# Kernel tuning notes

Measured on AMD Instinct MI355X. Metric: run time of the kernel, lower is better.

## Reference

```python
import jax, jax.numpy as jnp
import numpy as np

H = 8      # num_attention_heads
DH = 96    # attention_head_size
LN_EPS = 1e-5


def setup_inputs() -> dict:
    key = jax.random.key(0)
    ks = jax.random.split(key, 12)
    B, S, D = 2, 768, 768
    sc = 0.02
    return {
        "hidden_states": jax.random.normal(ks[0], (B, S, D), jnp.float32),
        "distance_matrix": jax.random.uniform(ks[1], (B, S, S), jnp.float32) * 20.0,
        "angle_matrix": jax.random.uniform(ks[2], (B, S, S), jnp.float32) * np.pi,
        "attention_mask": jnp.ones((B, S), jnp.float32),
        "Wq": jax.random.normal(ks[3], (D, D), jnp.float32) * sc,
        "bq": jnp.zeros((D,), jnp.float32),
        "Wk": jax.random.normal(ks[4], (D, D), jnp.float32) * sc,
        "bk": jnp.zeros((D,), jnp.float32),
        "Wv": jax.random.normal(ks[5], (D, D), jnp.float32) * sc,
        "bv": jnp.zeros((D,), jnp.float32),
        "Wd": jax.random.normal(ks[6], (DH,), jnp.float32) * sc,
        "bd": jnp.zeros((DH,), jnp.float32),
        "Wa": jax.random.normal(ks[7], (DH,), jnp.float32) * sc,
        "ba": jnp.zeros((DH,), jnp.float32),
        "Wo": jax.random.normal(ks[8], (D, D), jnp.float32) * sc,
        "bo": jnp.zeros((D,), jnp.float32),
        "ln_g": jnp.ones((D,), jnp.float32),
        "ln_b": jnp.zeros((D,), jnp.float32),
    }


def _heads(x, B, S):
    # [B,S,D] -> [B,H,S,DH]
    return x.reshape(B, S, H, DH).transpose(0, 2, 1, 3)


def reference(hidden_states, distance_matrix, angle_matrix, attention_mask,
              Wq, bq, Wk, bk, Wv, bv, Wd, bd, Wa, ba, Wo, bo, ln_g, ln_b):
    B, S, D = hidden_states.shape
    q = _heads(hidden_states @ Wq.T + bq, B, S)   # [B,H,S,DH]
    k = _heads(hidden_states @ Wk.T + bk, B, S)
    v = _heads(hidden_states @ Wv.T + bv, B, S)

    scores = jnp.einsum('bhid,bhjd->bhij', q, k) / jnp.sqrt(jnp.float32(DH))

    # distance / angle relative-position biases: emb[b,i,j,:] = dist[b,i,j]*Wd + bd
    dist_emb = distance_matrix[..., None] * Wd + bd   # [B,S,S,DH]
    scores = scores + jnp.einsum('bhid,bijd->bhij', q, dist_emb)
    ang_emb = angle_matrix[..., None] * Wa + ba       # [B,S,S,DH]
    scores = scores + jnp.einsum('bhid,bijd->bhij', q, ang_emb)

    # key mask, broadcast over heads and query positions
    scores = scores + (1.0 - attention_mask)[:, None, None, :] * -10000.0

    probs = jax.nn.softmax(scores, axis=-1)           # [B,H,S,S]
    ctx = jnp.einsum('bhij,bhjd->bhid', probs, v)
    ctx = ctx.transpose(0, 2, 1, 3).reshape(B, S, D)  # [B,S,D]

    out = ctx @ Wo.T + bo
    x = out + hidden_states
    mu = jnp.mean(x, axis=-1, keepdims=True)
    var = jnp.var(x, axis=-1, keepdims=True)
    out = (x - mu) * jax.lax.rsqrt(var + LN_EPS) * ln_g + ln_b
    return out, probs
```

## Files before the change

### kernel.cpp

```cpp
#include <hip/hip_runtime.h>
#include <stdint.h>

#define B_  2
#define S_  768
#define D_  768
#define H_  8
#define DH_ 96

typedef unsigned short ushort_t;
typedef __bf16 bf16x8 __attribute__((ext_vector_type(8)));
typedef float  f32x4  __attribute__((ext_vector_type(4)));
typedef _Float16 f16x4 __attribute__((ext_vector_type(4)));

__device__ inline ushort_t f2bf(float f) {
    union { float f; unsigned int u; } v; v.f = f;
    unsigned int u = v.u;
    unsigned int r = u + 0x7fffu + ((u >> 16) & 1u);
    return (ushort_t)(r >> 16);
}
__device__ inline float bf2f(ushort_t u) {
    union { unsigned int i; float f; } c; c.i = ((unsigned int)u) << 16;
    return c.f;
}
__device__ inline ushort_t f2h(float f) {
    union { _Float16 h; ushort_t u; } c; c.h = (_Float16)f; return c.u;
}

__device__ inline void glds16(const void* gp, void* lp) {
    auto g = reinterpret_cast<const __attribute__((address_space(1))) uint32_t*>(
        reinterpret_cast<uintptr_t>(gp));
    auto l = reinterpret_cast<__attribute__((address_space(3))) uint32_t*>(
        reinterpret_cast<uintptr_t>(lp));
    __builtin_amdgcn_global_load_lds(g, l, 16, 0, 0);
}

#define SBAR()  { __builtin_amdgcn_sched_barrier(0); __builtin_amdgcn_s_barrier(); \
                  __builtin_amdgcn_sched_barrier(0); }
#define WAIT_VM(N) { asm volatile("s_waitcnt vmcnt(" #N ")" ::: "memory"); \
                     __builtin_amdgcn_sched_barrier(0); }
#define WAIT_LGKM0() { asm volatile("s_waitcnt lgkmcnt(0)" ::: "memory"); \
                       __builtin_amdgcn_sched_barrier(0); }

__global__ __launch_bounds__(256) void k_convert(
        const float* __restrict__ X, const float* __restrict__ Wq,
        const float* __restrict__ Wk, const float* __restrict__ Wv,
        const float* __restrict__ Wo, const float* __restrict__ distm,
        const float* __restrict__ angm,
        ushort_t* __restrict__ Xb, ushort_t* __restrict__ Wb,
        ushort_t* __restrict__ Dh, ushort_t* __restrict__ Ah) {
    __shared__ float tlds[64][65];
    const int NX4 = (B_ * S_ * D_) / 4;
    const int NW4 = (D_ * D_) / 4;
    const int bid = blockIdx.x, tid = threadIdx.x;
    if (bid < 3456) {
        int i = bid * 256 + tid;
        float4 v;
        ushort_t* dst;
        if (i < NX4) {
            v = ((const float4*)X)[i];
            dst = Xb + i * 4;
        } else {
            int wi = i - NX4;
            int sel = wi / NW4;
            int off = wi - sel * NW4;
            const float* src = (sel == 0) ? Wq : (sel == 1) ? Wk : (sel == 2) ? Wv : Wo;
            v = ((const float4*)src)[off];
            dst = Wb + wi * 4;
        }
        ushort4 o;
        o.x = f2bf(v.x); o.y = f2bf(v.y); o.z = f2bf(v.z); o.w = f2bf(v.w);
        *(ushort4*)dst = o;
        return;
    }
    int tidx = bid - 3456;
    int mat = tidx / 288, t2 = tidx - mat * 288;
    int b = t2 / 144, t3 = t2 - b * 144;
    int rt = t3 / 12, ct = t3 - rt * 12;
    const float* src = (mat ? angm : distm) + ((size_t)(b * S_ + rt * 64)) * S_ + ct * 64;
    ushort_t* dstm = mat ? Ah : Dh;
    {
        int tr = tid >> 4, tc4 = tid & 15;
        #pragma unroll
        for (int k = 0; k < 4; ++k) {
            int row = tr + k * 16;
            float4 v4 = *(const float4*)(src + (size_t)row * S_ + tc4 * 4);
            tlds[row][tc4 * 4 + 0] = v4.x;
            tlds[row][tc4 * 4 + 1] = v4.y;
            tlds[row][tc4 * 4 + 2] = v4.z;
            tlds[row][tc4 * 4 + 3] = v4.w;
        }
    }
    __syncthreads();
    {
        int row = tid & 63, s4b = tid >> 6;
        #pragma unroll
        for (int k = 0; k < 4; ++k) {
            int s4l = s4b * 4 + k;
            ushort4 o4;
            o4.x = f2h(tlds[row][s4l * 4 + 0]);
            o4.y = f2h(tlds[row][s4l * 4 + 1]);
            o4.z = f2h(tlds[row][s4l * 4 + 2]);
            o4.w = f2h(tlds[row][s4l * 4 + 3]);
            *(ushort4*)&dstm[(((size_t)b * 192 + ct * 16 + s4l) * 768 + rt * 64 + row) * 4] = o4;
        }
    }
}

__device__ inline void gemm64_dbuf(
        const ushort_t* __restrict__ A, int lda,
        const ushort_t* __restrict__ Bt, int ldb,
        int K, int m0, int n0,
        ushort_t* As, ushort_t* Bs, f32x4 acc[2][2]) {
    const int tid  = threadIdx.x;
    const int lane = tid & 63, wave = tid >> 6;
    const int wm = (wave >> 1) * 32, wn = (wave & 1) * 32;
    const int fr = lane & 15, fk = (lane >> 4) * 8;
    const ushort_t* Ap = A  + (size_t)(m0 + wave * 16 + (lane >> 2)) * lda + (lane & 3) * 8;
    const ushort_t* Bp = Bt + (size_t)(n0 + wave * 16 + (lane >> 2)) * ldb + (lane & 3) * 8;
    glds16(Ap, As + wave * 512);
    glds16(Bp, Bs + wave * 512);
    for (int kt = 0; kt < K; kt += 32) {
        const int cur = (kt >> 5) & 1;
        if (kt + 32 < K) {
            glds16(Ap + kt + 32, As + (cur ^ 1) * 2048 + wave * 512);
            glds16(Bp + kt + 32, Bs + (cur ^ 1) * 2048 + wave * 512);
            WAIT_VM(2)
        } else {
            WAIT_VM(0)
        }
        SBAR()
        const ushort_t* Ab = As + cur * 2048;
        const ushort_t* Bb = Bs + cur * 2048;
        bf16x8 a0 = *(const bf16x8*)&Ab[(wm      + fr) * 32 + fk];
        bf16x8 a1 = *(const bf16x8*)&Ab[(wm + 16 + fr) * 32 + fk];
        bf16x8 b0 = *(const bf16x8*)&Bb[(wn      + fr) * 32 + fk];
        bf16x8 b1 = *(const bf16x8*)&Bb[(wn + 16 + fr) * 32 + fk];
        acc[0][0] = __builtin_amdgcn_mfma_f32_16x16x32_bf16(a0, b0, acc[0][0], 0, 0, 0);
        acc[0][1] = __builtin_amdgcn_mfma_f32_16x16x32_bf16(a0, b1, acc[0][1], 0, 0, 0);
        acc[1][0] = __builtin_amdgcn_mfma_f32_16x16x32_bf16(a1, b0, acc[1][0], 0, 0, 0);
        acc[1][1] = __builtin_amdgcn_mfma_f32_16x16x32_bf16(a1, b1, acc[1][1], 0, 0, 0);
        WAIT_LGKM0()
        SBAR()
    }
}

__global__ __launch_bounds__(256) void k_qkv(
        const ushort_t* __restrict__ Xb, const ushort_t* __restrict__ Wb,
        const float* __restrict__ bq, const float* __restrict__ bk,
        const float* __restrict__ bv,
        ushort_t* __restrict__ Qb, ushort_t* __restrict__ Kb,
        ushort_t* __restrict__ Vtb) {
    __shared__ __align__(16) ushort_t As[2 * 64 * 32];
    __shared__ __align__(16) ushort_t Bs[2 * 64 * 32];
    f32x4 acc[2][2];
    #pragma unroll
    for (int i = 0; i < 2; i++)
        #pragma unroll
        for (int j = 0; j < 2; j++) acc[i][j] = (f32x4){0.f, 0.f, 0.f, 0.f};
    const int m0 = blockIdx.y * 64, n0 = blockIdx.x * 64;
    gemm64_dbuf(Xb, D_, Wb, D_, D_, m0, n0, As, Bs, acc);
    const int lane = threadIdx.x & 63, wave = threadIdx.x >> 6;
    const int wm = (wave >> 1) * 32, wn = (wave & 1) * 32;
    #pragma unroll
    for (int ni = 0; ni < 2; ni++) {
        int gcol = n0 + wn + ni * 16 + (lane & 15);
        int gsel = gcol / D_, d768 = gcol - gsel * D_;
        int h = d768 / DH_, d = d768 - h * DH_;
        float bias = (gsel == 0 ? bq : (gsel == 1 ? bk : bv))[d768];
        #pragma unroll
        for (int mi = 0; mi < 2; mi++) {
            int grow0 = m0 + wm + mi * 16 + (lane >> 4) * 4;
            int b = grow0 / S_, s0 = grow0 - b * S_;
            int bh = b * H_ + h;
            if (gsel == 2) {
                ushort4 o4;
                o4.x = f2bf(acc[mi][ni][0] + bias);
                o4.y = f2bf(acc[mi][ni][1] + bias);
                o4.z = f2bf(acc[mi][ni][2] + bias);
                o4.w = f2bf(acc[mi][ni][3] + bias);
                int p = s0 >> 7, wv = (s0 >> 4) & 3, gq = (s0 >> 2) & 3;
                int e0 = (s0 >> 6) & 1;
                size_t off = ((size_t)bh * 73728) + p * 12288 + wv * 3072
                           + (d >> 4) * 512 + (gq * 16 + (d & 15)) * 8 + e0 * 4;
                *(ushort4*)&Vtb[off] = o4;
            } else if (gsel == 1) {
                #pragma unroll
                for (int r = 0; r < 4; r++)
                    Kb[(((size_t)bh * 12 + (d >> 3)) * S_ + s0 + r) * 8 + (d & 7)] =
                        f2bf(acc[mi][ni][r] + bias);
            } else {
                #pragma unroll
                for (int r = 0; r < 4; r++)
                    Qb[((size_t)bh * S_ + s0 + r) * DH_ + d] = f2bf(acc[mi][ni][r] + bias);
            }
        }
    }
}

__global__ __launch_bounds__(256, 3) void k_flash(
        const ushort_t* __restrict__ Qb, const ushort_t* __restrict__ Kb,
        const ushort_t* __restrict__ Vtb,
        const float* __restrict__ Wd, const float* __restrict__ bd,
        const float* __restrict__ Wa, const float* __restrict__ ba,
        const ushort_t* __restrict__ Dh, const ushort_t* __restrict__ Ah,
        const float* __restrict__ mask,
        float* __restrict__ probs, ushort_t* __restrict__ Ctxb) {
    __shared__ float mstat[64];
    __shared__ float lstat[64];
    __shared__ float ctxred[1600];
    const int idx = blockIdx.x;
    const int bh = idx & 15, t = idx >> 4;
    const int b = bh >> 3, h = bh & 7;
    const int r0 = t * 16;
    const int tid = threadIdx.x, lane = tid & 63, w = tid >> 6;
    const int frn = lane & 15, g = lane >> 4;
    const ushort_t* Qbh = Qb + (size_t)bh * S_ * DH_;
    const ushort_t* Kbh = Kb + (size_t)bh * 12 * S_ * 8;

    #pragma unroll
    for (int i = 0; i < 7; ++i) {
        int z = tid + i * 256;
        if (z < 1600) ctxred[z] = 0.f;
    }

    bf16x8 aq0, aq1, aq2;
    {
        const ushort_t* qp = Qbh + (size_t)(r0 + frn) * DH_ + g * 8;
        aq0 = *(const bf16x8*)qp;
        aq1 = *(const bf16x8*)(qp + 32);
        aq2 = *(const bf16x8*)(qp + 64);
    }
    float qc0 = 0.f, qc1 = 0.f, qc2 = 0.f;
    #pragma unroll
    for (int f = 0; f < 3; ++f) {
        bf16x8 aq = (f == 0) ? aq0 : (f == 1) ? aq1 : aq2;
        #pragma unroll
        for (int e = 0; e < 8; ++e) {
            int d = f * 32 + g * 8 + e;
            float qv = (float)aq[e];
            qc0 += qv * Wd[d];
            qc1 += qv * Wa[d];
            qc2 += qv * (bd[d] + ba[d]);
        }
    }
    qc0 += __shfl_xor(qc0, 16); qc0 += __shfl_xor(qc0, 32);
    qc1 += __shfl_xor(qc1, 16); qc1 += __shfl_xor(qc1, 32);
    qc2 += __shfl_xor(qc2, 16); qc2 += __shfl_xor(qc2, 32);

    const float isq = 0.10206207261596577f;

    f32x4 acc[12];
    const ushort_t* kbase = Kbh + ((size_t)g * S_ + 16 * w + frn) * 8;
    const ushort_t* dbase = Dh + ((size_t)(b * 192 + w * 4 + g) * 768 + r0 + frn) * 4;
    const ushort_t* abase = Ah + ((size_t)(b * 192 + w * 4 + g) * 768 + r0 + frn) * 4;
    const float*    mbase = mask + b * S_ + w * 16 + g * 4;
    #pragma unroll
    for (int c = 0; c < 12; ++c) {
        const ushort_t* kp = kbase + (size_t)c * 64 * 8;
        bf16x8 k0 = *(const bf16x8*)kp;
        bf16x8 k1 = *(const bf16x8*)(kp + (size_t)4 * S_ * 8);
        bf16x8 k2 = *(const bf16x8*)(kp + (size_t)8 * S_ * 8);
        union { uint2 u; f16x4 hh; } dd, aa;
        dd.u = *(const uint2*)(dbase + (size_t)c * 16 * 768 * 4);
        aa.u = *(const uint2*)(abase + (size_t)c * 16 * 768 * 4);
        float4 m4 = *(const float4*)(mbase + c * 64);
        f32x4 ca = (f32x4){0.f, 0.f, 0.f, 0.f};
        ca = __builtin_amdgcn_mfma_f32_16x16x32_bf16(k0, aq0, ca, 0, 0, 0);
        ca = __builtin_amdgcn_mfma_f32_16x16x32_bf16(k1, aq1, ca, 0, 0, 0);
        ca = __builtin_amdgcn_mfma_f32_16x16x32_bf16(k2, aq2, ca, 0, 0, 0);
        f32x4 o;
        o[0] = ca[0] * isq + (float)dd.hh[0] * qc0 + (float)aa.hh[0] * qc1 + qc2 + (1.f - m4.x) * -10000.f;
        o[1] = ca[1] * isq + (float)dd.hh[1] * qc0 + (float)aa.hh[1] * qc1 + qc2 + (1.f - m4.y) * -10000.f;
        o[2] = ca[2] * isq + (float)dd.hh[2] * qc0 + (float)aa.hh[2] * qc1 + qc2 + (1.f - m4.z) * -10000.f;
        o[3] = ca[3] * isq + (float)dd.hh[3] * qc0 + (float)aa.hh[3] * qc1 + qc2 + (1.f - m4.w) * -10000.f;
        acc[c] = o;
    }

    float mx = -1e30f;
    #pragma unroll
    for (int c = 0; c < 12; ++c)
        #pragma unroll
        for (int r = 0; r < 4; ++r) mx = fmaxf(mx, acc[c][r]);
    mx = fmaxf(mx, __shfl_xor(mx, 16));
    mx = fmaxf(mx, __shfl_xor(mx, 32));
    if (g == 0) mstat[w * 16 + frn] = mx;
    __syncthreads();
    float mf = fmaxf(fmaxf(mstat[frn], mstat[16 + frn]),
                     fmaxf(mstat[32 + frn], mstat[48 + frn]));
    float sum = 0.f;
    #pragma unroll
    for (int c = 0; c < 12; ++c)
        #pragma unroll
        for (int r = 0; r < 4; ++r) {
            float e = __expf(acc[c][r] - mf);
            acc[c][r] = e;
            sum += e;
        }
    sum += __shfl_xor(sum, 16);
    sum += __shfl_xor(sum, 32);
    if (g == 0) lstat[w * 16 + frn] = sum;
    __syncthreads();
    float inv = 1.f / (lstat[frn] + lstat[16 + frn] + lstat[32 + frn] + lstat[48 + frn]);

    f32x4 accO[6];
    #pragma unroll
    for (int i = 0; i < 6; ++i) accO[i] = (f32x4){0.f, 0.f, 0.f, 0.f};
    float* prow = probs + ((size_t)bh * S_ + r0 + frn) * S_ + w * 16 + g * 4;
    const ushort_t* vfb = Vtb + (size_t)bh * 73728 + w * 3072 + lane * 8;
    #pragma unroll
    for (int p = 0; p < 6; ++p) {
        const int c = 2 * p;
        bf16x8 vfrag[6];
        #pragma unroll
        for (int nt = 0; nt < 6; ++nt)
            vfrag[nt] = *(const bf16x8*)(vfb + p * 12288 + nt * 512);
        float4 pw;
        pw.x = acc[c][0] * inv; pw.y = acc[c][1] * inv;
        pw.z = acc[c][2] * inv; pw.w = acc[c][3] * inv;
        *(float4*)(prow + c * 64) = pw;
        pw.x = acc[c + 1][0] * inv; pw.y = acc[c + 1][1] * inv;
        pw.z = acc[c + 1][2] * inv; pw.w = acc[c + 1][3] * inv;
        *(float4*)(prow + (c + 1) * 64) = pw;
        union { bf16x8 v; ushort_t u[8]; } pa;
        #pragma unroll
        for (int r = 0; r < 4; ++r) {
            pa.u[r]     = f2bf(acc[c][r]);
            pa.u[r + 4] = f2bf(acc[c + 1][r]);
        }
        #pragma unroll
        for (int nt = 0; nt < 6; ++nt)
            accO[nt] = __builtin_amdgcn_mfma_f32_16x16x32_bf16(pa.v, vfrag[nt], accO[nt], 0, 0, 0);
    }

    #pragma unroll
    for (int nt = 0; nt < 6; ++nt)
        #pragma unroll
        for (int r = 0; r < 4; ++r)
            atomicAdd(&ctxred[(4 * g + r) * 100 + nt * 16 + frn], accO[nt][r]);
    __syncthreads();
    {
        int zr = tid >> 4, zc = tid & 15;
        float ivr = 1.f / (lstat[zr] + lstat[16 + zr] + lstat[32 + zr] + lstat[48 + zr]);
        ushort_t* crow = Ctxb + ((size_t)b * S_ + r0 + zr) * D_ + h * DH_;
        #pragma unroll
        for (int i = 0; i < 6; ++i)
            crow[i * 16 + zc] = f2bf(ctxred[zr * 100 + i * 16 + zc] * ivr);
    }
}

__global__ __launch_bounds__(256) void k_out(
        const ushort_t* __restrict__ Ctxb, const ushort_t* __restrict__ Wob,
        const float* __restrict__ bo, const float* __restrict__ hidden,
        float* __restrict__ xbuf) {
    __shared__ __align__(16) ushort_t As[2 * 64 * 32];
    __shared__ __align__(16) ushort_t Bs[2 * 64 * 32];
    f32x4 acc[2][2];
    #pragma unroll
    for (int i = 0; i < 2; i++)
        #pragma unroll
        for (int j = 0; j < 2; j++) acc[i][j] = (f32x4){0.f, 0.f, 0.f, 0.f};
    const int m0 = blockIdx.y * 64, n0 = blockIdx.x * 64;
    gemm64_dbuf(Ctxb, D_, Wob, D_, D_, m0, n0, As, Bs, acc);
    const int lane = threadIdx.x & 63, wave = threadIdx.x >> 6;
    const int wm = (wave >> 1) * 32, wn = (wave & 1) * 32;
    #pragma unroll
    for (int ni = 0; ni < 2; ni++) {
        int gcol = n0 + wn + ni * 16 + (lane & 15);
        float bias = bo[gcol];
        #pragma unroll
        for (int mi = 0; mi < 2; mi++) {
            #pragma unroll
            for (int r = 0; r < 4; r++) {
                int grow = m0 + wm + mi * 16 + (lane >> 4) * 4 + r;
                xbuf[(size_t)grow * D_ + gcol] =
                    acc[mi][ni][r] + bias + hidden[(size_t)grow * D_ + gcol];
            }
        }
    }
}

__global__ __launch_bounds__(256) void k_ln(
        const float* __restrict__ xbuf, const float* __restrict__ g,
        const float* __restrict__ bb, float* __restrict__ out) {
    const float* x = xbuf + (size_t)blockIdx.x * D_;
    const int t = threadIdx.x;
    float a0 = x[t], a1 = x[t + 256], a2 = x[t + 512];
    float s = a0 + a1 + a2;
    float ss = a0 * a0 + a1 * a1 + a2 * a2;
    __shared__ float r1[4], r2[4];
    #pragma unroll
    for (int o = 32; o > 0; o >>= 1) { s += __shfl_down(s, o); ss += __shfl_down(ss, o); }
    if ((t & 63) == 0) { r1[t >> 6] = s; r2[t >> 6] = ss; }
    __syncthreads();
    float ts = r1[0] + r1[1] + r1[2] + r1[3];
    float tss = r2[0] + r2[1] + r2[2] + r2[3];
    float mu = ts * (1.0f / D_);
    float var = tss * (1.0f / D_) - mu * mu;
    float rstd = rsqrtf(var + 1e-5f);
    float* o = out + (size_t)blockIdx.x * D_;
    o[t]       = (a0 - mu) * rstd * g[t]       + bb[t];
    o[t + 256] = (a1 - mu) * rstd * g[t + 256] + bb[t + 256];
    o[t + 512] = (a2 - mu) * rstd * g[t + 512] + bb[t + 512];
}

extern "C" void kernel_launch(void* const* d_in, const int* in_sizes, int n_in,
                              void* d_out, int out_size, void* d_ws, size_t ws_size,
                              hipStream_t stream) {
    const float* X     = (const float*)d_in[0];
    const float* distm = (const float*)d_in[1];
    const float* angm  = (const float*)d_in[2];
    const float* mask  = (const float*)d_in[3];
    const float* Wq    = (const float*)d_in[4];
    const float* bq    = (const float*)d_in[5];
    const float* Wk    = (const float*)d_in[6];
    const float* bk    = (const float*)d_in[7];
    const float* Wv    = (const float*)d_in[8];
    const float* bv    = (const float*)d_in[9];
    const float* Wd    = (const float*)d_in[10];
    const float* bd    = (const float*)d_in[11];
    const float* Wa    = (const float*)d_in[12];
    const float* ba    = (const float*)d_in[13];
    const float* Wo    = (const float*)d_in[14];
    const float* bo    = (const float*)d_in[15];
    const float* ln_g  = (const float*)d_in[16];
    const float* ln_b  = (const float*)d_in[17];

    float* outp  = (float*)d_out;
    float* probs = (float*)d_out + (size_t)B_ * S_ * D_;

    char* ws = (char*)d_ws;
    ushort_t* Xb    = (ushort_t*)(ws + 0);
    ushort_t* Wb    = (ushort_t*)(ws + 2359296);
    ushort_t* Qb    = (ushort_t*)(ws + 7077888);
    ushort_t* Kb    = (ushort_t*)(ws + 9437184);
    ushort_t* Vtb   = (ushort_t*)(ws + 11796480);
    ushort_t* Ctxb  = (ushort_t*)(ws + 14155776);
    float*    xbuf  = (float*)   (ws + 16662528);
    ushort_t* Dh    = (ushort_t*)(ws + 16662528);
    ushort_t* Ah    = (ushort_t*)(ws + 16662528 + 2359296);

    k_convert<<<4032, 256, 0, stream>>>(X, Wq, Wk, Wv, Wo, distm, angm, Xb, Wb, Dh, Ah);
    k_qkv<<<dim3(36, 24), 256, 0, stream>>>(Xb, Wb, bq, bk, bv, Qb, Kb, Vtb);
    k_flash<<<768, 256, 0, stream>>>(Qb, Kb, Vtb, Wd, bd, Wa, ba, Dh, Ah, mask, probs, Ctxb);
    k_out<<<dim3(12, 24), 256, 0, stream>>>(Ctxb, Wb + (size_t)2304 * 768, bo, X, xbuf);
    k_ln<<<1536, 256, 0, stream>>>(xbuf, ln_g, ln_b, outp);
}
```

Before: 182.5 us.

## Triple-buffer GEMM LDS staging and software-prefetch K/V fragments in attention

The shared GEMM helper moves from double to triple buffering in LDS. The next-next tile is issued after a single barrier, which removes the second per-iteration barrier and the lgkmcnt wait. The attention kernel now prefetches the K, distance, angle and mask fragments two chunks ahead and V fragments one chunk ahead in registers, and writes the probs output with nontemporal stores. The intent is to hide global-memory latency and reduce sync overhead, at the cost of more LDS and registers, which may lower occupancy.

```diff
diff --git a/kernel.cpp b/kernel.cpp
--- a/kernel.cpp
+++ b/kernel.cpp
@@ -38,8 +38,6 @@
                   __builtin_amdgcn_sched_barrier(0); }
 #define WAIT_VM(N) { asm volatile("s_waitcnt vmcnt(" #N ")" ::: "memory"); \
                      __builtin_amdgcn_sched_barrier(0); }
-#define WAIT_LGKM0() { asm volatile("s_waitcnt lgkmcnt(0)" ::: "memory"); \
-                       __builtin_amdgcn_sched_barrier(0); }
 
 __global__ __launch_bounds__(256) void k_convert(
         const float* __restrict__ X, const float* __restrict__ Wq,
@@ -106,7 +104,7 @@
     }
 }
 
-__device__ inline void gemm64_dbuf(
+__device__ inline void gemm64_tbuf(
         const ushort_t* __restrict__ A, int lda,
         const ushort_t* __restrict__ Bt, int ldb,
         int K, int m0, int n0,
@@ -117,18 +115,19 @@
     const int fr = lane & 15, fk = (lane >> 4) * 8;
     const ushort_t* Ap = A  + (size_t)(m0 + wave * 16 + (lane >> 2)) * lda + (lane & 3) * 8;
     const ushort_t* Bp = Bt + (size_t)(n0 + wave * 16 + (lane >> 2)) * ldb + (lane & 3) * 8;
-    glds16(Ap, As + wave * 512);
-    glds16(Bp, Bs + wave * 512);
+    glds16(Ap,      As + wave * 512);
+    glds16(Bp,      Bs + wave * 512);
+    glds16(Ap + 32, As + 2048 + wave * 512);
+    glds16(Bp + 32, Bs + 2048 + wave * 512);
     for (int kt = 0; kt < K; kt += 32) {
-        const int cur = (kt >> 5) & 1;
-        if (kt + 32 < K) {
-            glds16(Ap + kt + 32, As + (cur ^ 1) * 2048 + wave * 512);
-            glds16(Bp + kt + 32, Bs + (cur ^ 1) * 2048 + wave * 512);
-            WAIT_VM(2)
-        } else {
-            WAIT_VM(0)
-        }
+        const int cur = (kt >> 5) % 3;
+        if (kt + 32 < K) { WAIT_VM(2) } else { WAIT_VM(0) }
         SBAR()
+        if (kt + 64 < K) {
+            const int nb = ((kt >> 5) + 2) % 3;
+            glds16(Ap + kt + 64, As + nb * 2048 + wave * 512);
+            glds16(Bp + kt + 64, Bs + nb * 2048 + wave * 512);
+        }
         const ushort_t* Ab = As + cur * 2048;
         const ushort_t* Bb = Bs + cur * 2048;
         bf16x8 a0 = *(const bf16x8*)&Ab[(wm      + fr) * 32 + fk];
@@ -139,8 +138,6 @@
         acc[0][1] = __builtin_amdgcn_mfma_f32_16x16x32_bf16(a0, b1, acc[0][1], 0, 0, 0);
         acc[1][0] = __builtin_amdgcn_mfma_f32_16x16x32_bf16(a1, b0, acc[1][0], 0, 0, 0);
         acc[1][1] = __builtin_amdgcn_mfma_f32_16x16x32_bf16(a1, b1, acc[1][1], 0, 0, 0);
-        WAIT_LGKM0()
-        SBAR()
     }
 }
 
@@ -150,15 +147,15 @@
         const float* __restrict__ bv,
         ushort_t* __restrict__ Qb, ushort_t* __restrict__ Kb,
         ushort_t* __restrict__ Vtb) {
-    __shared__ __align__(16) ushort_t As[2 * 64 * 32];
-    __shared__ __align__(16) ushort_t Bs[2 * 64 * 32];
+    __shared__ __align__(16) ushort_t As[3 * 64 * 32];
+    __shared__ __align__(16) ushort_t Bs[3 * 64 * 32];
     f32x4 acc[2][2];
     #pragma unroll
     for (int i = 0; i < 2; i++)
         #pragma unroll
         for (int j = 0; j < 2; j++) acc[i][j] = (f32x4){0.f, 0.f, 0.f, 0.f};
     const int m0 = blockIdx.y * 64, n0 = blockIdx.x * 64;
-    gemm64_dbuf(Xb, D_, Wb, D_, D_, m0, n0, As, Bs, acc);
+    gemm64_tbuf(Xb, D_, Wb, D_, D_, m0, n0, As, Bs, acc);
     const int lane = threadIdx.x & 63, wave = threadIdx.x >> 6;
     const int wm = (wave >> 1) * 32, wn = (wave & 1) * 32;
     #pragma unroll
@@ -254,26 +251,36 @@
     const ushort_t* dbase = Dh + ((size_t)(b * 192 + w * 4 + g) * 768 + r0 + frn) * 4;
     const ushort_t* abase = Ah + ((size_t)(b * 192 + w * 4 + g) * 768 + r0 + frn) * 4;
     const float*    mbase = mask + b * S_ + w * 16 + g * 4;
+    struct Ch { bf16x8 k0, k1, k2; uint2 dd, aa; float4 m4; };
+    auto LDC = [&](int c) {
+        Ch r;
+        const ushort_t* kp = kbase + (size_t)c * 64 * 8;
+        r.k0 = *(const bf16x8*)kp;
+        r.k1 = *(const bf16x8*)(kp + (size_t)4 * S_ * 8);
+        r.k2 = *(const bf16x8*)(kp + (size_t)8 * S_ * 8);
+        r.dd = *(const uint2*)(dbase + (size_t)c * 16 * 768 * 4);
+        r.aa = *(const uint2*)(abase + (size_t)c * 16 * 768 * 4);
+        r.m4 = *(const float4*)(mbase + c * 64);
+        return r;
+    };
+    Ch p0 = LDC(0), p1 = LDC(1);
     #pragma unroll
     for (int c = 0; c < 12; ++c) {
-        const ushort_t* kp = kbase + (size_t)c * 64 * 8;
-        bf16x8 k0 = *(const bf16x8*)kp;
-        bf16x8 k1 = *(const bf16x8*)(kp + (size_t)4 * S_ * 8);
-        bf16x8 k2 = *(const bf16x8*)(kp + (size_t)8 * S_ * 8);
+        Ch nx;
+        if (c < 10) nx = LDC(c + 2); else nx = p1;
+        f32x4 ca = (f32x4){0.f, 0.f, 0.f, 0.f};
+        ca = __builtin_amdgcn_mfma_f32_16x16x32_bf16(p0.k0, aq0, ca, 0, 0, 0);
+        ca = __builtin_amdgcn_mfma_f32_16x16x32_bf16(p0.k1, aq1, ca, 0, 0, 0);
+        ca = __builtin_amdgcn_mfma_f32_16x16x32_bf16(p0.k2, aq2, ca, 0, 0, 0);
         union { uint2 u; f16x4 hh; } dd, aa;
-        dd.u = *(const uint2*)(dbase + (size_t)c * 16 * 768 * 4);
-        aa.u = *(const uint2*)(abase + (size_t)c * 16 * 768 * 4);
-        float4 m4 = *(const float4*)(mbase + c * 64);
-        f32x4 ca = (f32x4){0.f, 0.f, 0.f, 0.f};
-        ca = __builtin_amdgcn_mfma_f32_16x16x32_bf16(k0, aq0, ca, 0, 0, 0);
-        ca = __builtin_amdgcn_mfma_f32_16x16x32_bf16(k1, aq1, ca, 0, 0, 0);
-        ca = __builtin_amdgcn_mfma_f32_16x16x32_bf16(k2, aq2, ca, 0, 0, 0);
+        dd.u = p0.dd; aa.u = p0.aa;
         f32x4 o;
-        o[0] = ca[0] * isq + (float)dd.hh[0] * qc0 + (float)aa.hh[0] * qc1 + qc2 + (1.f - m4.x) * -10000.f;
-        o[1] = ca[1] * isq + (float)dd.hh[1] * qc0 + (float)aa.hh[1] * qc1 + qc2 + (1.f - m4.y) * -10000.f;
-        o[2] = ca[2] * isq + (float)dd.hh[2] * qc0 + (float)aa.hh[2] * qc1 + qc2 + (1.f - m4.z) * -10000.f;
-        o[3] = ca[3] * isq + (float)dd.hh[3] * qc0 + (float)aa.hh[3] * qc1 + qc2 + (1.f - m4.w) * -10000.f;
+        o[0] = ca[0] * isq + (float)dd.hh[0] * qc0 + (float)aa.hh[0] * qc1 + qc2 + (1.f - p0.m4.x) * -10000.f;
+        o[1] = ca[1] * isq + (float)dd.hh[1] * qc0 + (float)aa.hh[1] * qc1 + qc2 + (1.f - p0.m4.y) * -10000.f;
+        o[2] = ca[2] * isq + (float)dd.hh[2] * qc0 + (float)aa.hh[2] * qc1 + qc2 + (1.f - p0.m4.z) * -10000.f;
+        o[3] = ca[3] * isq + (float)dd.hh[3] * qc0 + (float)aa.hh[3] * qc1 + qc2 + (1.f - p0.m4.w) * -10000.f;
         acc[c] = o;
+        p0 = p1; p1 = nx;
     }
 
     float mx = -1e30f;
@@ -307,20 +314,25 @@
     for (int i = 0; i < 6; ++i) accO[i] = (f32x4){0.f, 0.f, 0.f, 0.f};
     float* prow = probs + ((size_t)bh * S_ + r0 + frn) * S_ + w * 16 + g * 4;
     const ushort_t* vfb = Vtb + (size_t)bh * 73728 + w * 3072 + lane * 8;
+    bf16x8 vcur[6];
+    #pragma unroll
+    for (int nt = 0; nt < 6; ++nt)
+        vcur[nt] = *(const bf16x8*)(vfb + nt * 512);
     #pragma unroll
     for (int p = 0; p < 6; ++p) {
         const int c = 2 * p;
-        bf16x8 vfrag[6];
+        bf16x8 vnx[6];
         #pragma unroll
         for (int nt = 0; nt < 6; ++nt)
-            vfrag[nt] = *(const bf16x8*)(vfb + p * 12288 + nt * 512);
-        float4 pw;
-        pw.x = acc[c][0] * inv; pw.y = acc[c][1] * inv;
-        pw.z = acc[c][2] * inv; pw.w = acc[c][3] * inv;
-        *(float4*)(prow + c * 64) = pw;
-        pw.x = acc[c + 1][0] * inv; pw.y = acc[c + 1][1] * inv;
-        pw.z = acc[c + 1][2] * inv; pw.w = acc[c + 1][3] * inv;
-        *(float4*)(prow + (c + 1) * 64) = pw;
+            vnx[nt] = (p < 5) ? *(const bf16x8*)(vfb + (p + 1) * 12288 + nt * 512)
+                              : vcur[nt];
+        f32x4 pw;
+        pw[0] = acc[c][0] * inv; pw[1] = acc[c][1] * inv;
+        pw[2] = acc[c][2] * inv; pw[3] = acc[c][3] * inv;
+        __builtin_nontemporal_store(pw, (f32x4*)(prow + c * 64));
+        pw[0] = acc[c + 1][0] * inv; pw[1] = acc[c + 1][1] * inv;
+        pw[2] = acc[c + 1][2] * inv; pw[3] = acc[c + 1][3] * inv;
+        __builtin_nontemporal_store(pw, (f32x4*)(prow + (c + 1) * 64));
         union { bf16x8 v; ushort_t u[8]; } pa;
         #pragma unroll
         for (int r = 0; r < 4; ++r) {
@@ -329,7 +341,9 @@
         }
         #pragma unroll
         for (int nt = 0; nt < 6; ++nt)
-            accO[nt] = __builtin_amdgcn_mfma_f32_16x16x32_bf16(pa.v, vfrag[nt], accO[nt], 0, 0, 0);
+            accO[nt] = __builtin_amdgcn_mfma_f32_16x16x32_bf16(pa.v, vcur[nt], accO[nt], 0, 0, 0);
+        #pragma unroll
+        for (int nt = 0; nt < 6; ++nt) vcur[nt] = vnx[nt];
     }
 
     #pragma unroll
@@ -352,15 +366,15 @@
         const ushort_t* __restrict__ Ctxb, const ushort_t* __restrict__ Wob,
         const float* __restrict__ bo, const float* __restrict__ hidden,
         float* __restrict__ xbuf) {
-    __shared__ __align__(16) ushort_t As[2 * 64 * 32];
-    __shared__ __align__(16) ushort_t Bs[2 * 64 * 32];
+    __shared__ __align__(16) ushort_t As[3 * 64 * 32];
+    __shared__ __align__(16) ushort_t Bs[3 * 64 * 32];
     f32x4 acc[2][2];
     #pragma unroll
     for (int i = 0; i < 2; i++)
         #pragma unroll
         for (int j = 0; j < 2; j++) acc[i][j] = (f32x4){0.f, 0.f, 0.f, 0.f};
     const int m0 = blockIdx.y * 64, n0 = blockIdx.x * 64;
-    gemm64_dbuf(Ctxb, D_, Wob, D_, D_, m0, n0, As, Bs, acc);
+    gemm64_tbuf(Ctxb, D_, Wob, D_, D_, m0, n0, As, Bs, acc);
     const int lane = threadIdx.x & 63, wave = threadIdx.x >> 6;
     const int wm = (wave >> 1) * 32, wn = (wave & 1) * 32;
     #pragma unroll
```

After: 179.3 us. Within noise of the previous version (-1.7%).
